# Optimization experiments

Measured on AMD Instinct MI355X. Metric: run time of the kernel, lower is better.

Reference implementation:

```python
import jax, jax.numpy as jnp
import numpy as np

NUM_HEADS = 4
LN_EPS = 1e-5
ALPHA_SCALE = 2.0


def setup_inputs() -> dict:
    key = jax.random.key(0)
    ks = jax.random.split(key, 8)
    bs, C, H, W = 64, 256, 56, 56
    T, D = 6, 192
    HW = H * W
    w = lambda k, shape: (jax.random.normal(k, shape, jnp.float32) * 0.02)
    return {
        "features": jax.random.normal(ks[0], (bs, C, H, W), jnp.float32),
        "tokens": jax.random.normal(ks[1], (T, bs, D), jnp.float32),
        # mlp: Linear(HW -> T)
        "mlp_w": w(ks[2], (T, HW)), "mlp_b": jnp.zeros((T,), jnp.float32),
        # q: Linear(D -> C)
        "q_w": w(ks[3], (C, D)), "q_b": jnp.zeros((C,), jnp.float32),
        # alpha: Linear(D -> C)
        "alpha_w": w(ks[4], (C, D)), "alpha_b": jnp.zeros((C,), jnp.float32),
        # proj: Linear(C -> D)
        "proj_w": w(ks[5], (D, C)), "proj_b": jnp.zeros((D,), jnp.float32),
        "ln_g": jnp.ones((D,), jnp.float32), "ln_b": jnp.zeros((D,), jnp.float32),
    }


def reference(features, tokens, mlp_w, mlp_b, q_w, q_b,
              alpha_w, alpha_b, proj_w, proj_b, ln_g, ln_b):
    bs, C, H, W = features.shape
    T, _, D = tokens.shape
    h = NUM_HEADS
    dh = C // h
    HW = H * W
    scale = dh ** -0.5

    f = features.reshape(bs, C, HW)

    # mlp branch: Linear over HW -> [bs, C, T] -> permute to [T, bs, C]
    t_sum = jnp.einsum('bcn,tn->tbc', f, mlp_w) + mlp_b[:, None, None]

    # attn branch: few tokens attend over H*W feature map (k reused as v)
    q = jnp.einsum('tbd,cd->tbc', tokens, q_w) + q_b          # [T, bs, C]
    q = q.reshape(T, bs, h, dh).transpose(1, 2, 0, 3)         # [bs, h, T, dh]
    k = f.reshape(bs, h, dh, HW)                              # [bs, h, dh, HW]
    attn = jnp.einsum('bhtd,bhdn->bhtn', q, k) * scale        # [bs, h, T, HW]
    a = jax.nn.softmax(attn, axis=-1)
    attn_out = jnp.einsum('bhtn,bhdn->bhtd', a, k)            # [bs, h, T, dh]
    t_a = attn_out.transpose(2, 0, 1, 3).reshape(T, bs, C)
    t_sum = t_sum + t_a

    # dynamic gate: h_sigmoid(alpha(tokens)) * 2.0
    alp = jnp.clip(jnp.einsum('tbd,cd->tbc', tokens, alpha_w) + alpha_b + 3.0,
                   0.0, 6.0) / 6.0 * ALPHA_SCALE              # [T, bs, C]
    t_sum = t_sum * alp

    # proj + residual + LayerNorm (post-norm, drop_path rate 0 -> identity)
    t_sum = jnp.einsum('tbc,dc->tbd', t_sum, proj_w) + proj_b  # [T, bs, D]
    tok = tokens + t_sum
    mu = tok.mean(-1, keepdims=True)
    var = ((tok - mu) ** 2).mean(-1, keepdims=True)
    tok = (tok - mu) * jax.lax.rsqrt(var + LN_EPS) * ln_g + ln_b

    return tok, attn.reshape(bs, h, T, H, W)
```

## Files before the change

kernel.cpp:

```cpp
#include <hip/hip_runtime.h>
#include <hip/hip_bf16.h>

constexpr int BS = 64, C = 256, NH = 4, DH = 64, T = 6, D = 192;
constexpr int HW = 3136;
constexpr int NT = 112;
constexpr int S = 7, CPB = 4;
constexpr int PNT = 116;
constexpr float SCALE = 0.125f;
constexpr float LN_EPS = 1e-5f;

__global__ __launch_bounds__(256) void qalpha_kernel(
    const float* __restrict__ tokens,
    const float* __restrict__ q_w,
    const float* __restrict__ q_b,
    const float* __restrict__ alpha_w,
    const float* __restrict__ alpha_b,
    float* __restrict__ q_ws,
    float* __restrict__ alp_ws)
{
    int b = blockIdx.x;
    int c = threadIdx.x;
    __shared__ float tok_s[T][D];
    for (int i = c; i < T * (D / 4); i += 256) {
        int t = i / (D / 4), v = i % (D / 4);
        *(float4*)&tok_s[t][4 * v] =
            *(const float4*)&tokens[((size_t)t * BS + b) * D + 4 * v];
    }
    __syncthreads();

    const float4* qr = (const float4*)(q_w + (size_t)c * D);
    const float4* ar = (const float4*)(alpha_w + (size_t)c * D);
    float accq[T] = {0, 0, 0, 0, 0, 0};
    float acca[T] = {0, 0, 0, 0, 0, 0};
    for (int v = 0; v < D / 4; ++v) {
        float4 qw4 = qr[v], aw4 = ar[v];
#pragma unroll
        for (int t = 0; t < T; ++t) {
            float4 t4 = *(const float4*)&tok_s[t][4 * v];
            accq[t] += qw4.x * t4.x + qw4.y * t4.y + qw4.z * t4.z + qw4.w * t4.w;
            acca[t] += aw4.x * t4.x + aw4.y * t4.y + aw4.z * t4.z + aw4.w * t4.w;
        }
    }
    float qb = q_b[c], ab = alpha_b[c];
#pragma unroll
    for (int t = 0; t < T; ++t) {
        size_t idx = ((size_t)t * BS + b) * C + c;
        q_ws[idx] = accq[t] + qb;
        float aa = acca[t] + ab + 3.0f;
        alp_ws[idx] = fminf(fmaxf(aa, 0.0f), 6.0f) * (2.0f / 6.0f);
    }
}

__global__ __launch_bounds__(384) void fused_attn_mlp(
    const float* __restrict__ feat,
    const float* __restrict__ mlp_w,
    const float* __restrict__ q_ws,
    float* __restrict__ out_attn,
    float* __restrict__ o_part,
    float* __restrict__ mlp_part,
    float* __restrict__ ml_part)
{
    int bh = blockIdx.x / S, sp = blockIdx.x % S;
    int b = bh / NH, h = bh % NH;
    int tid = threadIdx.x;
    int wave = tid >> 6, lane = tid & 63;

    __shared__ float qs[T][DH];
    __shared__ float fch[DH][PNT];
    __shared__ float st[T][PNT];
    __shared__ float pp[T][PNT];
    __shared__ float mww[T][PNT];
    __shared__ float m_s[T], l_s[T];
    __shared__ float al_s[8];

    for (int i = tid; i < T * DH; i += 384) {
        int t = i / DH, c2 = i % DH;
        qs[t][c2] = q_ws[((size_t)t * BS + b) * C + h * DH + c2];
    }
    if (tid < T) { m_s[tid] = -3e38f; l_s[tid] = 0.f; }

    const float* fbase = feat + ((size_t)b * C + h * DH) * HW;
    float* obase = out_attn + ((size_t)bh * T) * HW;

    float O_p[T] = {0, 0, 0, 0, 0, 0};
    float M_p[T] = {0, 0, 0, 0, 0, 0};

    const int s_t = tid / 56, s_n = 2 * (tid % 56);

    __syncthreads();

    for (int cc = 0; cc < CPB; ++cc) {
        const int n0 = (sp * CPB + cc) * NT;
        for (int i = tid; i < DH * (NT / 4); i += 384) {
            int c2 = i / (NT / 4), v = i % (NT / 4);
            *(float4*)&fch[c2][4 * v] =
                *(const float4*)&fbase[(size_t)c2 * HW + n0 + 4 * v];
        }
        for (int i = tid; i < T * (NT / 4); i += 384) {
            int t = i / (NT / 4), v = i % (NT / 4);
            *(float4*)&mww[t][4 * v] =
                *(const float4*)&mlp_w[(size_t)t * HW + n0 + 4 * v];
        }
        __syncthreads();

        if (tid < 336) {
            float ax = 0.f, ay = 0.f;
#pragma unroll 4
            for (int cq = 0; cq < DH / 4; ++cq) {
                float4 q4 = *(const float4*)&qs[s_t][4 * cq];
                float2 f0 = *(const float2*)&fch[4 * cq + 0][s_n];
                float2 f1 = *(const float2*)&fch[4 * cq + 1][s_n];
                float2 f2 = *(const float2*)&fch[4 * cq + 2][s_n];
                float2 f3 = *(const float2*)&fch[4 * cq + 3][s_n];
                ax += q4.x * f0.x + q4.y * f1.x + q4.z * f2.x + q4.w * f3.x;
                ay += q4.x * f0.y + q4.y * f1.y + q4.z * f2.y + q4.w * f3.y;
            }
            ax *= SCALE; ay *= SCALE;
            st[s_t][s_n] = ax; st[s_t][s_n + 1] = ay;
            *(float2*)&obase[(size_t)s_t * HW + n0 + s_n] = make_float2(ax, ay);
        }
        __syncthreads();

        {
            int t = wave;
            float mloc = -3e38f;
            for (int n = lane; n < NT; n += 64) mloc = fmaxf(mloc, st[t][n]);
#pragma unroll
            for (int off = 32; off; off >>= 1) mloc = fmaxf(mloc, __shfl_down(mloc, off));
            mloc = __shfl(mloc, 0);
            float m_old = m_s[t], m_new = fmaxf(m_old, mloc);
            float ssum = 0.f;
            for (int n = lane; n < NT; n += 64) {
                float p = __expf(st[t][n] - m_new);
                pp[t][n] = p;
                ssum += p;
            }
#pragma unroll
            for (int off = 32; off; off >>= 1) ssum += __shfl_down(ssum, off);
            if (lane == 0) {
                float alpha = __expf(m_old - m_new);
                l_s[t] = l_s[t] * alpha + ssum;
                m_s[t] = m_new;
                al_s[t] = alpha;
            }
        }
        __syncthreads();

        {
            float4 a03 = *(const float4*)&al_s[0];
            float al4 = al_s[4], al5 = al_s[5];
            O_p[0] *= a03.x; O_p[1] *= a03.y; O_p[2] *= a03.z; O_p[3] *= a03.w;
            O_p[4] *= al4;   O_p[5] *= al5;
            for (int nq = wave; nq < NT / 4; nq += 6) {
                float4 f4 = *(const float4*)&fch[lane][4 * nq];
#pragma unroll
                for (int t = 0; t < T; ++t) {
                    float4 p4 = *(const float4*)&pp[t][4 * nq];
                    float4 w4 = *(const float4*)&mww[t][4 * nq];
                    O_p[t] += p4.x * f4.x + p4.y * f4.y + p4.z * f4.z + p4.w * f4.w;
                    M_p[t] += w4.x * f4.x + w4.y * f4.y + w4.z * f4.z + w4.w * f4.w;
                }
            }
        }
        __syncthreads();
    }

    float* red = &fch[0][0];
    float* red_o = red;
    float* red_m = red + 6 * T * DH;
#pragma unroll
    for (int t = 0; t < T; ++t) {
        red_o[(wave * T + t) * DH + lane] = O_p[t];
        red_m[(wave * T + t) * DH + lane] = M_p[t];
    }
    __syncthreads();

    {
        int t = wave;
        float o = 0.f, m = 0.f;
#pragma unroll
        for (int w = 0; w < 6; ++w) {
            o += red_o[(w * T + t) * DH + lane];
            m += red_m[(w * T + t) * DH + lane];
        }
        size_t pidx = ((size_t)blockIdx.x * T + t) * DH + lane;
        o_part[pidx] = o;
        mlp_part[pidx] = m;
    }
    if (tid < 2 * T) {
        int t = tid >> 1;
        ml_part[((size_t)blockIdx.x * T + t) * 2 + (tid & 1)] =
            (tid & 1) ? l_s[t] : m_s[t];
    }
}

__global__ __launch_bounds__(256) void merge_proj_ln_kernel(
    const float* __restrict__ o_part,
    const float* __restrict__ mlp_part,
    const float* __restrict__ ml_part,
    const float* __restrict__ mlp_b,
    const float* __restrict__ alp_ws,
    const float* __restrict__ tokens,
    const float* __restrict__ proj_w,
    const float* __restrict__ proj_b,
    const float* __restrict__ ln_g,
    const float* __restrict__ ln_b,
    float* __restrict__ out_tok)
{
    int tb = blockIdx.x;
    int t = tb / BS, b = tb % BS;
    int tid = threadIdx.x;
    __shared__ float g_s[C];
    __shared__ float r1[4], r2[4];

    {
        int c = tid;
        int h = c >> 6, cl = c & 63;
        int bh = b * NH + h;
        float m[S], l[S];
        float M = -3e38f;
#pragma unroll
        for (int s = 0; s < S; ++s) {
            size_t blk = (size_t)(bh * S + s);
            m[s] = ml_part[(blk * T + t) * 2 + 0];
            l[s] = ml_part[(blk * T + t) * 2 + 1];
            M = fmaxf(M, m[s]);
        }
        float L = 0.f, O = 0.f, MLP = 0.f;
#pragma unroll
        for (int s = 0; s < S; ++s) {
            float w = __expf(m[s] - M);
            size_t blk = (size_t)(bh * S + s);
            size_t pidx = (blk * T + t) * DH + cl;
            L += l[s] * w;
            O += o_part[pidx] * w;
            MLP += mlp_part[pidx];
        }
        size_t idx = (size_t)tb * C + c;
        g_s[c] = (MLP + mlp_b[t] + O / L) * alp_ws[idx];
    }
    __syncthreads();

    if (tid < D) {
        int d = tid;
        float acc = proj_b[d] + tokens[(size_t)tb * D + d];
        const float4* pr = (const float4*)(proj_w + (size_t)d * C);
#pragma unroll 8
        for (int v = 0; v < C / 4; ++v) {
            float4 w4 = pr[v];
            float4 g4 = *(const float4*)&g_s[4 * v];
            acc += w4.x * g4.x + w4.y * g4.y + w4.z * g4.z + w4.w * g4.w;
        }

        float s1 = acc, s2 = acc * acc;
#pragma unroll
        for (int off = 32; off; off >>= 1) { s1 += __shfl_down(s1, off); s2 += __shfl_down(s2, off); }
        int wv = d >> 6, lane = d & 63;
        if (lane == 0) { r1[wv] = s1; r2[wv] = s2; }
        __syncthreads();
        float sum1 = r1[0] + r1[1] + r1[2];
        float sum2 = r2[0] + r2[1] + r2[2];
        float mu = sum1 * (1.0f / D);
        float var = sum2 * (1.0f / D) - mu * mu;
        float inv = rsqrtf(var + LN_EPS);
        out_tok[(size_t)tb * D + d] = (acc - mu) * inv * ln_g[d] + ln_b[d];
    } else {
        __syncthreads();
    }
}

extern "C" void kernel_launch(void* const* d_in, const int* in_sizes, int n_in,
                              void* d_out, int out_size, void* d_ws, size_t ws_size,
                              hipStream_t stream) {
    const float* features = (const float*)d_in[0];
    const float* tokens   = (const float*)d_in[1];
    const float* mlp_w    = (const float*)d_in[2];
    const float* mlp_b    = (const float*)d_in[3];
    const float* q_w      = (const float*)d_in[4];
    const float* q_b      = (const float*)d_in[5];
    const float* alpha_w  = (const float*)d_in[6];
    const float* alpha_b  = (const float*)d_in[7];
    const float* proj_w   = (const float*)d_in[8];
    const float* proj_b   = (const float*)d_in[9];
    const float* ln_g     = (const float*)d_in[10];
    const float* ln_b     = (const float*)d_in[11];

    float* out_tok  = (float*)d_out;
    float* out_attn = (float*)d_out + T * BS * D;

    constexpr int NBLK = BS * NH * S;
    float* q_ws     = (float*)d_ws;
    float* alp_ws   = q_ws + T * BS * C;
    float* ml_part  = alp_ws + T * BS * C;
    float* o_part   = ml_part + NBLK * T * 2;
    float* mlp_part = o_part + NBLK * T * DH;

    qalpha_kernel<<<BS, 256, 0, stream>>>(
        tokens, q_w, q_b, alpha_w, alpha_b, q_ws, alp_ws);

    fused_attn_mlp<<<NBLK, 384, 0, stream>>>(
        features, mlp_w, q_ws, out_attn, o_part, mlp_part, ml_part);

    merge_proj_ln_kernel<<<T * BS, 256, 0, stream>>>(
        o_part, mlp_part, ml_part, mlp_b, alp_ws, tokens,
        proj_w, proj_b, ln_g, ln_b, out_tok);
}
```

Measured before the change: 391.7 us.

## Use bf16 MFMA for score and PV/MLP products in fused attention kernel

Converts the feature chunk, q, mlp weights and softmax probabilities to bf16 in shared memory. The QK^T scores and the combined P·F / W·F accumulation now run on 16x16x32 bf16 MFMA instructions instead of scalar FP32 FMAs. This also removes the per-wave register partials and the final cross-wave shared-memory reduction. Precision drops to bf16 for the attention logits and accumulation inputs, which may matter for tolerance on the returned attention map.

```diff
diff --git a/kernel.cpp b/kernel.cpp
--- a/kernel.cpp
+++ b/kernel.cpp
@@ -5,9 +5,20 @@
 constexpr int HW = 3136;
 constexpr int NT = 112;
 constexpr int S = 7, CPB = 4;
-constexpr int PNT = 116;
+constexpr int PNF = 136;
+constexpr int PNS = 116;
+constexpr int QP = 72;
 constexpr float SCALE = 0.125f;
 constexpr float LN_EPS = 1e-5f;
+
+typedef short bf16x8 __attribute__((ext_vector_type(8)));
+typedef float f32x4 __attribute__((ext_vector_type(4)));
+
+__device__ inline unsigned short f2bf(float x) {
+    union { float f; unsigned u; } v; v.f = x;
+    unsigned r = v.u + 0x7FFFu + ((v.u >> 16) & 1u);
+    return (unsigned short)(r >> 16);
+}
 
 __global__ __launch_bounds__(256) void qalpha_kernel(
     const float* __restrict__ tokens,
@@ -64,77 +75,82 @@
     int b = bh / NH, h = bh % NH;
     int tid = threadIdx.x;
     int wave = tid >> 6, lane = tid & 63;
-
-    __shared__ float qs[T][DH];
-    __shared__ float fch[DH][PNT];
-    __shared__ float st[T][PNT];
-    __shared__ float pp[T][PNT];
-    __shared__ float mww[T][PNT];
-    __shared__ float m_s[T], l_s[T];
-    __shared__ float al_s[8];
-
+    int col = lane & 15, quad = lane >> 4;
+
+    __shared__ unsigned short fch[DH][PNF];
+    __shared__ unsigned short pw[16][PNF];
+    __shared__ unsigned short qs[16][QP];
+    __shared__ float st[T][PNS];
+    __shared__ float m_s[T], l_s[T], al_s[T];
+
+    for (int i = tid; i < 16 * PNF; i += 384) pw[i / PNF][i % PNF] = 0;
+    for (int i = tid; i < DH * 24; i += 384) fch[i / 24][112 + (i % 24)] = 0;
+    for (int i = tid; i < 16 * QP; i += 384) qs[i / QP][i % QP] = 0;
+    if (tid < T) { m_s[tid] = -3e38f; l_s[tid] = 0.f; }
+    __syncthreads();
     for (int i = tid; i < T * DH; i += 384) {
         int t = i / DH, c2 = i % DH;
-        qs[t][c2] = q_ws[((size_t)t * BS + b) * C + h * DH + c2];
-    }
-    if (tid < T) { m_s[tid] = -3e38f; l_s[tid] = 0.f; }
+        qs[t][c2] = f2bf(q_ws[((size_t)t * BS + b) * C + h * DH + c2]);
+    }
 
     const float* fbase = feat + ((size_t)b * C + h * DH) * HW;
     float* obase = out_attn + ((size_t)bh * T) * HW;
 
-    float O_p[T] = {0, 0, 0, 0, 0, 0};
-    float M_p[T] = {0, 0, 0, 0, 0, 0};
-
-    const int s_t = tid / 56, s_n = 2 * (tid % 56);
-
+    f32x4 accPW = {0.f, 0.f, 0.f, 0.f};
     __syncthreads();
 
     for (int cc = 0; cc < CPB; ++cc) {
         const int n0 = (sp * CPB + cc) * NT;
         for (int i = tid; i < DH * (NT / 4); i += 384) {
             int c2 = i / (NT / 4), v = i % (NT / 4);
-            *(float4*)&fch[c2][4 * v] =
-                *(const float4*)&fbase[(size_t)c2 * HW + n0 + 4 * v];
+            float4 f4 = *(const float4*)&fbase[(size_t)c2 * HW + n0 + 4 * v];
+            unsigned lo = (unsigned)f2bf(f4.x) | ((unsigned)f2bf(f4.y) << 16);
+            unsigned hi = (unsigned)f2bf(f4.z) | ((unsigned)f2bf(f4.w) << 16);
+            *(uint2*)&fch[c2][4 * v] = make_uint2(lo, hi);
         }
         for (int i = tid; i < T * (NT / 4); i += 384) {
             int t = i / (NT / 4), v = i % (NT / 4);
-            *(float4*)&mww[t][4 * v] =
-                *(const float4*)&mlp_w[(size_t)t * HW + n0 + 4 * v];
-        }
-        __syncthreads();
-
-        if (tid < 336) {
-            float ax = 0.f, ay = 0.f;
-#pragma unroll 4
-            for (int cq = 0; cq < DH / 4; ++cq) {
-                float4 q4 = *(const float4*)&qs[s_t][4 * cq];
-                float2 f0 = *(const float2*)&fch[4 * cq + 0][s_n];
-                float2 f1 = *(const float2*)&fch[4 * cq + 1][s_n];
-                float2 f2 = *(const float2*)&fch[4 * cq + 2][s_n];
-                float2 f3 = *(const float2*)&fch[4 * cq + 3][s_n];
-                ax += q4.x * f0.x + q4.y * f1.x + q4.z * f2.x + q4.w * f3.x;
-                ay += q4.x * f0.y + q4.y * f1.y + q4.z * f2.y + q4.w * f3.y;
-            }
-            ax *= SCALE; ay *= SCALE;
-            st[s_t][s_n] = ax; st[s_t][s_n + 1] = ay;
-            *(float2*)&obase[(size_t)s_t * HW + n0 + s_n] = make_float2(ax, ay);
+            float4 f4 = *(const float4*)&mlp_w[(size_t)t * HW + n0 + 4 * v];
+            unsigned lo = (unsigned)f2bf(f4.x) | ((unsigned)f2bf(f4.y) << 16);
+            unsigned hi = (unsigned)f2bf(f4.z) | ((unsigned)f2bf(f4.w) << 16);
+            *(uint2*)&pw[6 + t][4 * v] = make_uint2(lo, hi);
+        }
+        __syncthreads();
+
+        for (int tile = wave; tile < 7; tile += 6) {
+            bf16x8 a0 = *(const bf16x8*)&qs[col][quad * 8];
+            bf16x8 a1 = *(const bf16x8*)&qs[col][32 + quad * 8];
+            bf16x8 b0, b1;
+#pragma unroll
+            for (int j = 0; j < 8; ++j) {
+                b0[j] = (short)fch[quad * 8 + j][tile * 16 + col];
+                b1[j] = (short)fch[32 + quad * 8 + j][tile * 16 + col];
+            }
+            f32x4 acc = {0.f, 0.f, 0.f, 0.f};
+            acc = __builtin_amdgcn_mfma_f32_16x16x32_bf16(a0, b0, acc, 0, 0, 0);
+            acc = __builtin_amdgcn_mfma_f32_16x16x32_bf16(a1, b1, acc, 0, 0, 0);
+#pragma unroll
+            for (int reg = 0; reg < 4; ++reg) {
+                int r = quad * 4 + reg;
+                if (r < 6) st[r][tile * 16 + col] = acc[reg] * SCALE;
+            }
         }
         __syncthreads();
 
         {
             int t = wave;
-            float mloc = -3e38f;
-            for (int n = lane; n < NT; n += 64) mloc = fmaxf(mloc, st[t][n]);
+            float v0 = st[t][lane];
+            float v1 = (lane + 64 < NT) ? st[t][lane + 64] : -3e38f;
+            float mloc = fmaxf(v0, v1);
 #pragma unroll
             for (int off = 32; off; off >>= 1) mloc = fmaxf(mloc, __shfl_down(mloc, off));
             mloc = __shfl(mloc, 0);
             float m_old = m_s[t], m_new = fmaxf(m_old, mloc);
-            float ssum = 0.f;
-            for (int n = lane; n < NT; n += 64) {
-                float p = __expf(st[t][n] - m_new);
-                pp[t][n] = p;
-                ssum += p;
-            }
+            float p0 = __expf(v0 - m_new);
+            float p1 = (lane + 64 < NT) ? __expf(v1 - m_new) : 0.f;
+            pw[t][lane] = f2bf(p0);
+            if (lane + 64 < NT) pw[t][lane + 64] = f2bf(p1);
+            float ssum = p0 + p1;
 #pragma unroll
             for (int off = 32; off; off >>= 1) ssum += __shfl_down(ssum, off);
             if (lane == 0) {
@@ -143,49 +159,36 @@
                 m_s[t] = m_new;
                 al_s[t] = alpha;
             }
-        }
-        __syncthreads();
-
-        {
-            float4 a03 = *(const float4*)&al_s[0];
-            float al4 = al_s[4], al5 = al_s[5];
-            O_p[0] *= a03.x; O_p[1] *= a03.y; O_p[2] *= a03.z; O_p[3] *= a03.w;
-            O_p[4] *= al4;   O_p[5] *= al5;
-            for (int nq = wave; nq < NT / 4; nq += 6) {
-                float4 f4 = *(const float4*)&fch[lane][4 * nq];
-#pragma unroll
-                for (int t = 0; t < T; ++t) {
-                    float4 p4 = *(const float4*)&pp[t][4 * nq];
-                    float4 w4 = *(const float4*)&mww[t][4 * nq];
-                    O_p[t] += p4.x * f4.x + p4.y * f4.y + p4.z * f4.z + p4.w * f4.w;
-                    M_p[t] += w4.x * f4.x + w4.y * f4.y + w4.z * f4.z + w4.w * f4.w;
-                }
-            }
-        }
-        __syncthreads();
-    }
-
-    float* red = &fch[0][0];
-    float* red_o = red;
-    float* red_m = red + 6 * T * DH;
-#pragma unroll
-    for (int t = 0; t < T; ++t) {
-        red_o[(wave * T + t) * DH + lane] = O_p[t];
-        red_m[(wave * T + t) * DH + lane] = M_p[t];
-    }
-    __syncthreads();
-
-    {
-        int t = wave;
-        float o = 0.f, m = 0.f;
-#pragma unroll
-        for (int w = 0; w < 6; ++w) {
-            o += red_o[(w * T + t) * DH + lane];
-            m += red_m[(w * T + t) * DH + lane];
-        }
-        size_t pidx = ((size_t)blockIdx.x * T + t) * DH + lane;
-        o_part[pidx] = o;
-        mlp_part[pidx] = m;
+            if (lane < NT / 4) {
+                *(float4*)&obase[(size_t)t * HW + n0 + 4 * lane] =
+                    *(const float4*)&st[t][4 * lane];
+            }
+        }
+        __syncthreads();
+
+        if (wave < 4) {
+            float alpha = (col < 6) ? al_s[col] : 1.0f;
+            accPW *= alpha;
+#pragma unroll
+            for (int ks = 0; ks < 4; ++ks) {
+                bf16x8 af = *(const bf16x8*)&fch[wave * 16 + col][ks * 32 + quad * 8];
+                bf16x8 bf = *(const bf16x8*)&pw[col][ks * 32 + quad * 8];
+                accPW = __builtin_amdgcn_mfma_f32_16x16x32_bf16(af, bf, accPW, 0, 0, 0);
+            }
+        }
+        __syncthreads();
+    }
+
+    if (wave < 4) {
+#pragma unroll
+        for (int reg = 0; reg < 4; ++reg) {
+            int c2 = wave * 16 + quad * 4 + reg;
+            if (col < 6) {
+                o_part[((size_t)blockIdx.x * T + col) * DH + c2] = accPW[reg];
+            } else if (col < 12) {
+                mlp_part[((size_t)blockIdx.x * T + (col - 6)) * DH + c2] = accPW[reg];
+            }
+        }
     }
     if (tid < 2 * T) {
         int t = tid >> 1;
```

Measured after the change: 357.6 us. 8.7% less time.
